# Kernel tuning notes

Measured on AMD Instinct MI355X. Metric: run time of the kernel, lower is better.

## Reference

```python
import jax, jax.numpy as jnp
import numpy as np

B, T, C = 2, 2048, 2048
N_HEAD = 16
HD = C // N_HEAD  # 128


def setup_inputs() -> dict:
    key = jax.random.key(0)
    k1, k2, k3, k4, k5 = jax.random.split(key, 5)
    s_in = 1.0 / np.sqrt(C)
    return {
        "x": jax.random.normal(k1, (B, T, C), dtype=jnp.float32),
        # weights stored as (in, out), i.e. transpose of torch Linear weight
        "W_attn": jax.random.normal(k2, (C, 3 * C), dtype=jnp.float32) * s_in,
        "b_attn": jax.random.normal(k3, (3 * C,), dtype=jnp.float32) * 0.02,
        "W_proj": jax.random.normal(k4, (C, C), dtype=jnp.float32) * s_in,
        "b_proj": jax.random.normal(k5, (C,), dtype=jnp.float32) * 0.02,
    }


def reference(x, W_attn, b_attn, W_proj, b_proj):
    # qkv projection: (B,T,3C)
    qkv = x @ W_attn + b_attn
    q, k, v = jnp.split(qkv, 3, axis=-1)
    # (B, n_head, T, head_dim)
    q = q.reshape(B, T, N_HEAD, HD).transpose(0, 2, 1, 3)
    k = k.reshape(B, T, N_HEAD, HD).transpose(0, 2, 1, 3)
    v = v.reshape(B, T, N_HEAD, HD).transpose(0, 2, 1, 3)
    # scores (B,H,T,T), causal mask (T_q == T_k prefill path)
    att = jnp.einsum("bhqd,bhkd->bhqk", q, k) * (1.0 / np.sqrt(HD))
    causal = jnp.tril(jnp.ones((T, T), dtype=bool))
    att = jnp.where(causal[None, None], att, -jnp.inf)
    att = jax.nn.softmax(att, axis=-1)  # attn_dropout is identity (p=0)
    y = jnp.einsum("bhqk,bhkd->bhqd", att, v)
    y = y.transpose(0, 2, 1, 3).reshape(B, T, C)
    y = y @ W_proj + b_proj  # resid_dropout identity (p=0)
    # new_cache = (k, v, T) since T == block_size; return output tensor
    return y
```

## Files before the change

kernel.cpp:

```cpp
#include <hip/hip_runtime.h>
#include <cstdint>
#include <cstddef>


typedef __bf16 bf16x8 __attribute__((ext_vector_type(8)));
typedef float  f32x4  __attribute__((ext_vector_type(4)));

__device__ __forceinline__ unsigned short f2bf(float f) {
  unsigned int u = __builtin_bit_cast(unsigned int, f);
  u += 0x7fffu + ((u >> 16) & 1u);
  return (unsigned short)(u >> 16);
}

__device__ __forceinline__ void gld16(void* lds, const void* g) {
  __builtin_amdgcn_global_load_lds(
      (const __attribute__((address_space(1))) void*)g,
      (__attribute__((address_space(3))) void*)lds, 16, 0, 0);
}

__global__ void cvt_f32_bf16_k(const float* __restrict__ in,
                               unsigned short* __restrict__ out, int n4) {
  int i = blockIdx.x * blockDim.x + threadIdx.x;
  int stride = gridDim.x * blockDim.x;
  for (; i < n4; i += stride) {
    float4 v = ((const float4*)in)[i];
    ushort4 o;
    o.x = f2bf(v.x); o.y = f2bf(v.y); o.z = f2bf(v.z); o.w = f2bf(v.w);
    ((ushort4*)out)[i] = o;
  }
}

__global__ void transpose_f32_bf16(const float* __restrict__ in,
                                   unsigned short* __restrict__ out,
                                   int R, int C) {
  __shared__ float tile[32][33];
  int c0 = blockIdx.x * 32, r0 = blockIdx.y * 32;
  int tx = threadIdx.x, ty = threadIdx.y;
#pragma unroll
  for (int i = 0; i < 4; i++)
    tile[ty + i * 8][tx] = in[(size_t)(r0 + ty + i * 8) * C + c0 + tx];
  __syncthreads();
#pragma unroll
  for (int i = 0; i < 4; i++)
    out[(size_t)(c0 + ty + i * 8) * R + r0 + tx] = f2bf(tile[tx][ty + i * 8]);
}

__global__ void extract_vT_k(const unsigned short* __restrict__ qkv,
                             unsigned short* __restrict__ vT) {
  __shared__ unsigned short tile[32][33];
  int bh = blockIdx.z;
  int b = bh >> 4, h = bh & 15;
  int t0 = blockIdx.x * 32, d0 = blockIdx.y * 32;
  int tx = threadIdx.x, ty = threadIdx.y;
  const unsigned short* src = qkv + (size_t)(b * 2048) * 6144 + 4096 + h * 128;
#pragma unroll
  for (int i = 0; i < 4; i++)
    tile[ty + i * 8][tx] = src[(size_t)(t0 + ty + i * 8) * 6144 + d0 + tx];
  __syncthreads();
  unsigned short* dst = vT + (size_t)bh * 128 * 2048;
#pragma unroll
  for (int i = 0; i < 4; i++)
    dst[(size_t)(d0 + ty + i * 8) * 2048 + t0 + tx] = tile[tx][ty + i * 8];
}

template <int OUT_BF16>
__global__ __launch_bounds__(256) void gemm_bt(
    const unsigned short* __restrict__ A, const unsigned short* __restrict__ BT,
    const float* __restrict__ bias, void* __restrict__ Cout,
    int M, int N, int K) {
  __shared__ __align__(16) unsigned short sA[128 * 32];
  __shared__ __align__(16) unsigned short sB[128 * 32];

  const int tid = threadIdx.x, w = tid >> 6, lane = tid & 63;
  const int quad = lane >> 4, l16 = lane & 15;
  const int m0 = blockIdx.y * 128, n0 = blockIdx.x * 128;
  const int wr = w >> 1, wc = w & 1;

  const int c0 = w * 128 + lane;
  const int c1 = w * 128 + 64 + lane;
  const unsigned short* gA0 = A + (size_t)(m0 + (c0 >> 2)) * K + (c0 & 3) * 8;
  const unsigned short* gA1 = A + (size_t)(m0 + (c1 >> 2)) * K + (c1 & 3) * 8;
  const unsigned short* gB0 = BT + (size_t)(n0 + (c0 >> 2)) * K + (c0 & 3) * 8;
  const unsigned short* gB1 = BT + (size_t)(n0 + (c1 >> 2)) * K + (c1 & 3) * 8;
  unsigned short* lA0 = sA + (size_t)(w * 128) * 8;
  unsigned short* lA1 = sA + (size_t)(w * 128 + 64) * 8;
  unsigned short* lB0 = sB + (size_t)(w * 128) * 8;
  unsigned short* lB1 = sB + (size_t)(w * 128 + 64) * 8;

  f32x4 acc[4][4] = {};

  for (int k0 = 0; k0 < K; k0 += 32) {
    gld16(lA0, gA0); gld16(lA1, gA1);
    gld16(lB0, gB0); gld16(lB1, gB1);
    gA0 += 32; gA1 += 32; gB0 += 32; gB1 += 32;
    __syncthreads();

    bf16x8 af[4], bfr[4];
#pragma unroll
    for (int mi = 0; mi < 4; mi++)
      af[mi] = *(const bf16x8*)&sA[(wr * 64 + mi * 16 + l16) * 32 + quad * 8];
#pragma unroll
    for (int ni = 0; ni < 4; ni++)
      bfr[ni] = *(const bf16x8*)&sB[(wc * 64 + ni * 16 + l16) * 32 + quad * 8];
#pragma unroll
    for (int mi = 0; mi < 4; mi++)
#pragma unroll
      for (int ni = 0; ni < 4; ni++)
        acc[mi][ni] = __builtin_amdgcn_mfma_f32_16x16x32_bf16(
            af[mi], bfr[ni], acc[mi][ni], 0, 0, 0);
    __syncthreads();
  }

#pragma unroll
  for (int mi = 0; mi < 4; mi++) {
    int row = m0 + wr * 64 + mi * 16 + quad * 4;
#pragma unroll
    for (int ni = 0; ni < 4; ni++) {
      int col = n0 + wc * 64 + ni * 16 + l16;
      float bv = bias[col];
#pragma unroll
      for (int r = 0; r < 4; r++) {
        float v = acc[mi][ni][r] + bv;
        if (OUT_BF16)
          ((unsigned short*)Cout)[(size_t)(row + r) * N + col] = f2bf(v);
        else
          ((float*)Cout)[(size_t)(row + r) * N + col] = v;
      }
    }
  }
}

__global__ __launch_bounds__(256) void flash_attn(
    const unsigned short* __restrict__ qkv, const unsigned short* __restrict__ vT,
    unsigned short* __restrict__ yout) {
  __shared__ __align__(16) unsigned short sK[2][64 * 128];
  __shared__ __align__(16) unsigned short sVT[2][128 * 64];
  __shared__ __align__(16) unsigned short sP[4 * 16 * 64];

  const int tid = threadIdx.x, w = tid >> 6, lane = tid & 63;
  const int quad = lane >> 4, l16 = lane & 15;
  const int id = blockIdx.x;
  const int g = id & 31;
  const int qp = id >> 5;
  const int b = g >> 4, h = g & 15;
  const int T = 2048, CC = 6144, HD = 128;
  const float qscale = 0.12753257252f;

  const unsigned short* gK = qkv + (size_t)(b * T) * CC + 2048 + h * HD;
  const unsigned short* gV = vT + (size_t)(b * 16 + h) * HD * T;
  unsigned short* pw = sP + w * 16 * 64;

  const unsigned short* kSrc[4];
  const unsigned short* vSrc[4];
  unsigned short* kDst[4];
  unsigned short* vDst[4];
#pragma unroll
  for (int i = 0; i < 4; i++) {
    int c = w * 256 + i * 64 + lane;
    int kR = c >> 4, kC = (c & 15) ^ (kR & 15);
    int vR = c >> 3, vC = (c & 7) ^ (vR & 7);
    kSrc[i] = gK + (size_t)kR * CC + kC * 8;
    vSrc[i] = gV + (size_t)vR * T + vC * 8;
    kDst[i] = (unsigned short*)sK + (size_t)(w * 256 + i * 64) * 8;
    vDst[i] = (unsigned short*)sVT + (size_t)(w * 256 + i * 64) * 8;
  }
  const int KBUF = 64 * 128, VBUF = 128 * 64;

  const int qtA = qp, qtB = 31 - qp;
  int qt = qtA, kt = 0;

  bf16x8 qf[4];
  float m_old[4], l_sum[4];
  f32x4 o[8] = {};
  {
    const size_t qrow = (size_t)(b * T + qt * 64 + w * 16 + l16) * CC + h * HD;
#pragma unroll
    for (int kb = 0; kb < 4; kb++) {
      bf16x8 raw = *(const bf16x8*)&qkv[qrow + kb * 32 + quad * 8];
      bf16x8 sc;
#pragma unroll
      for (int j = 0; j < 8; j++) sc[j] = (__bf16)((float)raw[j] * qscale);
      qf[kb] = sc;
    }
  }
#pragma unroll
  for (int r = 0; r < 4; r++) { m_old[r] = -1e30f; l_sum[r] = 0.f; }

#pragma unroll
  for (int i = 0; i < 4; i++) {
    gld16(kDst[i], kSrc[i]);
    gld16(vDst[i], vSrc[i]);
  }

  const int total = qtA + qtB + 2;
  for (int it = 0; it < total; ++it) {
    __syncthreads();
    const int cur = it & 1;
    const bool segEnd = (kt == qt);

    if (it + 1 < total) {
      const int nkt = segEnd ? 0 : kt + 1;
      const int nb_ = (it + 1) & 1;
      const size_t kOff = (size_t)nkt * 64 * CC;
      const int vOff = nkt * 64;
#pragma unroll
      for (int i = 0; i < 4; i++) {
        gld16(kDst[i] + (size_t)nb_ * KBUF * 8 / 8, kSrc[i] + kOff);
        gld16(vDst[i] + (size_t)nb_ * VBUF, vSrc[i] + vOff);
      }
    }

    const unsigned short* sKc = (const unsigned short*)sK + (size_t)cur * KBUF;
    const unsigned short* sVc = (const unsigned short*)sVT + (size_t)cur * VBUF;
    f32x4 s4[4] = {};
#pragma unroll
    for (int kb = 0; kb < 4; kb++) {
#pragma unroll
      for (int cb = 0; cb < 4; cb++) {
        int rr = cb * 16 + l16;
        int cc = (kb * 4 + quad) ^ l16;
        bf16x8 kf = *(const bf16x8*)&sKc[rr * 128 + cc * 8];
        s4[cb] = __builtin_amdgcn_mfma_f32_16x16x32_bf16(qf[kb], kf, s4[cb], 0, 0, 0);
      }
    }

    float sv[4][4];
#pragma unroll
    for (int cb = 0; cb < 4; cb++)
#pragma unroll
      for (int r = 0; r < 4; r++) {
        float v = s4[cb][r];
        if (segEnd) {
          int col = cb * 16 + l16;
          int row = w * 16 + quad * 4 + r;
          if (col > row) v = -1e30f;
        }
        sv[cb][r] = v;
      }

    float alpha[4];
#pragma unroll
    for (int r = 0; r < 4; r++) {
      float mx = fmaxf(fmaxf(sv[0][r], sv[1][r]), fmaxf(sv[2][r], sv[3][r]));
#pragma unroll
      for (int off = 8; off >= 1; off >>= 1) mx = fmaxf(mx, __shfl_xor(mx, off, 16));
      float m_new = fmaxf(m_old[r], mx);
      float a = exp2f(m_old[r] - m_new);
      float ssum = 0.f;
#pragma unroll
      for (int cb = 0; cb < 4; cb++) {
        float p = exp2f(sv[cb][r] - m_new);
        sv[cb][r] = p;
        ssum += p;
      }
#pragma unroll
      for (int off = 8; off >= 1; off >>= 1) ssum += __shfl_xor(ssum, off, 16);
      l_sum[r] = l_sum[r] * a + ssum;
      m_old[r] = m_new;
      alpha[r] = a;
    }

#pragma unroll
    for (int nb = 0; nb < 8; nb++)
#pragma unroll
      for (int r = 0; r < 4; r++) o[nb][r] *= alpha[r];

#pragma unroll
    for (int cb = 0; cb < 4; cb++) {
#pragma unroll
      for (int r = 0; r < 4; r++) {
        int prow = quad * 4 + r;
        int pcol = cb * 16 + l16;
        int pcc = (pcol >> 3) ^ (prow & 7);
        pw[prow * 64 + pcc * 8 + (pcol & 7)] = f2bf(sv[cb][r]);
      }
    }

#pragma unroll
    for (int kb2 = 0; kb2 < 2; kb2++) {
      int pcc = (kb2 * 4 + quad) ^ (l16 & 7);
      bf16x8 pf = *(const bf16x8*)&pw[l16 * 64 + pcc * 8];
#pragma unroll
      for (int nb = 0; nb < 8; nb++) {
        int rr = nb * 16 + l16;
        int cc = (kb2 * 4 + quad) ^ (rr & 7);
        bf16x8 vf = *(const bf16x8*)&sVc[rr * 64 + cc * 8];
        o[nb] = __builtin_amdgcn_mfma_f32_16x16x32_bf16(pf, vf, o[nb], 0, 0, 0);
      }
    }

    if (segEnd) {
#pragma unroll
      for (int r = 0; r < 4; r++) {
        float inv = 1.0f / l_sum[r];
        size_t orow = (size_t)(b * T + qt * 64 + w * 16 + quad * 4 + r) * 2048 + h * HD;
#pragma unroll
        for (int nb = 0; nb < 8; nb++)
          yout[orow + nb * 16 + l16] = f2bf(o[nb][r] * inv);
      }
      if (it + 1 < total) {
        qt = qtB;
        const size_t qrow = (size_t)(b * T + qt * 64 + w * 16 + l16) * CC + h * HD;
#pragma unroll
        for (int kb = 0; kb < 4; kb++) {
          bf16x8 raw = *(const bf16x8*)&qkv[qrow + kb * 32 + quad * 8];
          bf16x8 sc;
#pragma unroll
          for (int j = 0; j < 8; j++) sc[j] = (__bf16)((float)raw[j] * qscale);
          qf[kb] = sc;
        }
#pragma unroll
        for (int r = 0; r < 4; r++) { m_old[r] = -1e30f; l_sum[r] = 0.f; }
#pragma unroll
        for (int nb = 0; nb < 8; nb++) o[nb] = (f32x4){0.f, 0.f, 0.f, 0.f};
      }
      kt = 0;
    } else {
      kt++;
    }
  }
}

extern "C" void kernel_launch(void* const* d_in, const int* in_sizes, int n_in,
                              void* d_out, int out_size, void* d_ws, size_t ws_size,
                              hipStream_t stream) {
  const float* x      = (const float*)d_in[0];
  const float* W_attn = (const float*)d_in[1];
  const float* b_attn = (const float*)d_in[2];
  const float* W_proj = (const float*)d_in[3];
  const float* b_proj = (const float*)d_in[4];
  float* out = (float*)d_out;

  char* ws = (char*)d_ws;
  unsigned short* x_bf  = (unsigned short*)(ws);
  unsigned short* WaT   = (unsigned short*)(ws + 16777216);
  unsigned short* WpT   = (unsigned short*)(ws + 41943040);
  unsigned short* qkv   = (unsigned short*)(ws + 50331648);
  unsigned short* vT    = (unsigned short*)(ws + 100663296);
  unsigned short* y_att = (unsigned short*)(ws + 117440512);

  cvt_f32_bf16_k<<<1024, 256, 0, stream>>>(x, x_bf, 8388608 / 4);
  transpose_f32_bf16<<<dim3(192, 64), dim3(32, 8), 0, stream>>>(W_attn, WaT, 2048, 6144);
  transpose_f32_bf16<<<dim3(64, 64), dim3(32, 8), 0, stream>>>(W_proj, WpT, 2048, 2048);
  gemm_bt<1><<<dim3(48, 32), 256, 0, stream>>>(x_bf, WaT, b_attn, qkv, 4096, 6144, 2048);
  extract_vT_k<<<dim3(64, 4, 32), dim3(32, 8), 0, stream>>>(qkv, vT);
  flash_attn<<<dim3(512), 256, 0, stream>>>(qkv, vT, y_att);
  gemm_bt<0><<<dim3(16, 32), 256, 0, stream>>>(y_att, WpT, b_proj, out, 4096, 2048, 2048);
}
```

Before: 440.3 us.

## Widen GEMM K-tile with swizzled LDS, vectorize transposes, transpose S in attention

The GEMM now stages 64-wide K tiles through XOR-swizzled LDS, which halves the number of barriers per K and is meant to reduce bank conflicts. The weight-transpose and V-extract kernels move to 64x64 tiles with vectorized 16-byte global loads and stores. Flash attention computes S transposed (K as the A operand), so each lane owns one query row: the softmax reductions need only two cross-lane shuffles, and P is written to LDS as packed 4-element stores. The cost is extra shuffles to broadcast alpha and 1/l back to the row layout, plus more LDS per GEMM block.

```diff
diff --git a/kernel.cpp b/kernel.cpp
--- a/kernel.cpp
+++ b/kernel.cpp
@@ -5,6 +5,8 @@
 
 typedef __bf16 bf16x8 __attribute__((ext_vector_type(8)));
 typedef float  f32x4  __attribute__((ext_vector_type(4)));
+typedef unsigned short u16x4 __attribute__((ext_vector_type(4)));
+typedef unsigned short u16x8 __attribute__((ext_vector_type(8)));
 
 __device__ __forceinline__ unsigned short f2bf(float f) {
   unsigned int u = __builtin_bit_cast(unsigned int, f);
@@ -30,37 +32,62 @@
   }
 }
 
-__global__ void transpose_f32_bf16(const float* __restrict__ in,
-                                   unsigned short* __restrict__ out,
-                                   int R, int C) {
-  __shared__ float tile[32][33];
-  int c0 = blockIdx.x * 32, r0 = blockIdx.y * 32;
-  int tx = threadIdx.x, ty = threadIdx.y;
-#pragma unroll
-  for (int i = 0; i < 4; i++)
-    tile[ty + i * 8][tx] = in[(size_t)(r0 + ty + i * 8) * C + c0 + tx];
+__global__ __launch_bounds__(256) void transpose_f32_bf16(
+    const float* __restrict__ in, unsigned short* __restrict__ out,
+    int R, int C) {
+  __shared__ float tile[64][65];
+  int c0 = blockIdx.x * 64, r0 = blockIdx.y * 64;
+  int t = threadIdx.x;
+  int lr = t >> 4, lc = (t & 15) * 4;
+#pragma unroll
+  for (int i = 0; i < 4; i++) {
+    int row = lr + i * 16;
+    float4 v = *(const float4*)&in[(size_t)(r0 + row) * C + c0 + lc];
+    tile[row][lc] = v.x; tile[row][lc + 1] = v.y;
+    tile[row][lc + 2] = v.z; tile[row][lc + 3] = v.w;
+  }
   __syncthreads();
-#pragma unroll
-  for (int i = 0; i < 4; i++)
-    out[(size_t)(c0 + ty + i * 8) * R + r0 + tx] = f2bf(tile[tx][ty + i * 8]);
-}
-
-__global__ void extract_vT_k(const unsigned short* __restrict__ qkv,
-                             unsigned short* __restrict__ vT) {
-  __shared__ unsigned short tile[32][33];
-  int bh = blockIdx.z;
-  int b = bh >> 4, h = bh & 15;
-  int t0 = blockIdx.x * 32, d0 = blockIdx.y * 32;
-  int tx = threadIdx.x, ty = threadIdx.y;
+  int wr = t >> 3, wc = (t & 7) * 8;
+#pragma unroll
+  for (int i = 0; i < 2; i++) {
+    int crow = wr + i * 32;
+    u16x8 o;
+#pragma unroll
+    for (int j = 0; j < 8; j++) o[j] = f2bf(tile[wc + j][crow]);
+    *(u16x8*)&out[(size_t)(c0 + crow) * R + r0 + wc] = o;
+  }
+}
+
+__global__ __launch_bounds__(256) void extract_vT_k(
+    const unsigned short* __restrict__ qkv, unsigned short* __restrict__ vT) {
+  __shared__ unsigned int tile32[64][33];
+  int bh = blockIdx.z, b = bh >> 4, h = bh & 15;
+  int t0 = blockIdx.x * 64, d0 = blockIdx.y * 64;
+  int t = threadIdx.x;
+  int lr = t >> 3, lc = (t & 7) * 8;
   const unsigned short* src = qkv + (size_t)(b * 2048) * 6144 + 4096 + h * 128;
 #pragma unroll
-  for (int i = 0; i < 4; i++)
-    tile[ty + i * 8][tx] = src[(size_t)(t0 + ty + i * 8) * 6144 + d0 + tx];
+  for (int i = 0; i < 2; i++) {
+    int row = lr + i * 32;
+    u16x8 v = *(const u16x8*)&src[(size_t)(t0 + row) * 6144 + d0 + lc];
+#pragma unroll
+    for (int j = 0; j < 8; j++) {
+      unsigned short* p = (unsigned short*)&tile32[lc + j][row & 31];
+      p[row >> 5] = v[j];
+    }
+  }
   __syncthreads();
-  unsigned short* dst = vT + (size_t)bh * 128 * 2048;
-#pragma unroll
-  for (int i = 0; i < 4; i++)
-    dst[(size_t)(d0 + ty + i * 8) * 2048 + t0 + tx] = tile[tx][ty + i * 8];
+  int dr = t >> 2, tc = (t & 3) * 8;
+  u16x8 lo, hi;
+#pragma unroll
+  for (int j = 0; j < 8; j++) {
+    unsigned int u = tile32[dr][tc + j];
+    lo[j] = (unsigned short)(u & 0xffffu);
+    hi[j] = (unsigned short)(u >> 16);
+  }
+  unsigned short* dst = vT + (size_t)bh * 128 * 2048 + (size_t)(d0 + dr) * 2048 + t0;
+  *(u16x8*)&dst[tc] = lo;
+  *(u16x8*)&dst[tc + 32] = hi;
 }
 
 template <int OUT_BF16>
@@ -68,46 +95,55 @@
     const unsigned short* __restrict__ A, const unsigned short* __restrict__ BT,
     const float* __restrict__ bias, void* __restrict__ Cout,
     int M, int N, int K) {
-  __shared__ __align__(16) unsigned short sA[128 * 32];
-  __shared__ __align__(16) unsigned short sB[128 * 32];
+  __shared__ __align__(16) unsigned short sA[128 * 64];
+  __shared__ __align__(16) unsigned short sB[128 * 64];
 
   const int tid = threadIdx.x, w = tid >> 6, lane = tid & 63;
   const int quad = lane >> 4, l16 = lane & 15;
   const int m0 = blockIdx.y * 128, n0 = blockIdx.x * 128;
   const int wr = w >> 1, wc = w & 1;
 
-  const int c0 = w * 128 + lane;
-  const int c1 = w * 128 + 64 + lane;
-  const unsigned short* gA0 = A + (size_t)(m0 + (c0 >> 2)) * K + (c0 & 3) * 8;
-  const unsigned short* gA1 = A + (size_t)(m0 + (c1 >> 2)) * K + (c1 & 3) * 8;
-  const unsigned short* gB0 = BT + (size_t)(n0 + (c0 >> 2)) * K + (c0 & 3) * 8;
-  const unsigned short* gB1 = BT + (size_t)(n0 + (c1 >> 2)) * K + (c1 & 3) * 8;
-  unsigned short* lA0 = sA + (size_t)(w * 128) * 8;
-  unsigned short* lA1 = sA + (size_t)(w * 128 + 64) * 8;
-  unsigned short* lB0 = sB + (size_t)(w * 128) * 8;
-  unsigned short* lB1 = sB + (size_t)(w * 128 + 64) * 8;
+  const unsigned short* gA[4];
+  const unsigned short* gB[4];
+  unsigned short* lA[4];
+  unsigned short* lB[4];
+#pragma unroll
+  for (int i = 0; i < 4; i++) {
+    int c = w * 256 + i * 64 + lane;
+    int row = c >> 3, scol = (c & 7) ^ (row & 7);
+    gA[i] = A + (size_t)(m0 + row) * K + scol * 8;
+    gB[i] = BT + (size_t)(n0 + row) * K + scol * 8;
+    lA[i] = sA + (size_t)(w * 256 + i * 64) * 8;
+    lB[i] = sB + (size_t)(w * 256 + i * 64) * 8;
+  }
 
   f32x4 acc[4][4] = {};
 
-  for (int k0 = 0; k0 < K; k0 += 32) {
-    gld16(lA0, gA0); gld16(lA1, gA1);
-    gld16(lB0, gB0); gld16(lB1, gB1);
-    gA0 += 32; gA1 += 32; gB0 += 32; gB1 += 32;
+  for (int k0 = 0; k0 < K; k0 += 64) {
+#pragma unroll
+    for (int i = 0; i < 4; i++) {
+      gld16(lA[i], gA[i]); gld16(lB[i], gB[i]);
+      gA[i] += 64; gB[i] += 64;
+    }
     __syncthreads();
 
-    bf16x8 af[4], bfr[4];
-#pragma unroll
-    for (int mi = 0; mi < 4; mi++)
-      af[mi] = *(const bf16x8*)&sA[(wr * 64 + mi * 16 + l16) * 32 + quad * 8];
-#pragma unroll
-    for (int ni = 0; ni < 4; ni++)
-      bfr[ni] = *(const bf16x8*)&sB[(wc * 64 + ni * 16 + l16) * 32 + quad * 8];
-#pragma unroll
-    for (int mi = 0; mi < 4; mi++)
+#pragma unroll
+    for (int kk = 0; kk < 2; kk++) {
+      const int cc = (kk * 4 + quad) ^ (l16 & 7);
+      bf16x8 af[4], bfr[4];
+#pragma unroll
+      for (int mi = 0; mi < 4; mi++)
+        af[mi] = *(const bf16x8*)&sA[(wr * 64 + mi * 16 + l16) * 64 + cc * 8];
 #pragma unroll
       for (int ni = 0; ni < 4; ni++)
-        acc[mi][ni] = __builtin_amdgcn_mfma_f32_16x16x32_bf16(
-            af[mi], bfr[ni], acc[mi][ni], 0, 0, 0);
+        bfr[ni] = *(const bf16x8*)&sB[(wc * 64 + ni * 16 + l16) * 64 + cc * 8];
+#pragma unroll
+      for (int mi = 0; mi < 4; mi++)
+#pragma unroll
+        for (int ni = 0; ni < 4; ni++)
+          acc[mi][ni] = __builtin_amdgcn_mfma_f32_16x16x32_bf16(
+              af[mi], bfr[ni], acc[mi][ni], 0, 0, 0);
+    }
     __syncthreads();
   }
 
@@ -170,7 +206,7 @@
   int qt = qtA, kt = 0;
 
   bf16x8 qf[4];
-  float m_old[4], l_sum[4];
+  float m_old, l_sum;
   f32x4 o[8] = {};
   {
     const size_t qrow = (size_t)(b * T + qt * 64 + w * 16 + l16) * CC + h * HD;
@@ -183,8 +219,7 @@
       qf[kb] = sc;
     }
   }
-#pragma unroll
-  for (int r = 0; r < 4; r++) { m_old[r] = -1e30f; l_sum[r] = 0.f; }
+  m_old = -1e30f; l_sum = 0.f;
 
 #pragma unroll
   for (int i = 0; i < 4; i++) {
@@ -205,75 +240,78 @@
       const int vOff = nkt * 64;
 #pragma unroll
       for (int i = 0; i < 4; i++) {
-        gld16(kDst[i] + (size_t)nb_ * KBUF * 8 / 8, kSrc[i] + kOff);
+        gld16(kDst[i] + (size_t)nb_ * KBUF, kSrc[i] + kOff);
         gld16(vDst[i] + (size_t)nb_ * VBUF, vSrc[i] + vOff);
       }
     }
 
     const unsigned short* sKc = (const unsigned short*)sK + (size_t)cur * KBUF;
     const unsigned short* sVc = (const unsigned short*)sVT + (size_t)cur * VBUF;
+
     f32x4 s4[4] = {};
 #pragma unroll
+    for (int dc = 0; dc < 4; dc++) {
+#pragma unroll
+      for (int kb = 0; kb < 4; kb++) {
+        int rr = kb * 16 + l16;
+        int cc = (dc * 4 + quad) ^ l16;
+        bf16x8 kf = *(const bf16x8*)&sKc[rr * 128 + cc * 8];
+        s4[kb] = __builtin_amdgcn_mfma_f32_16x16x32_bf16(kf, qf[dc], s4[kb], 0, 0, 0);
+      }
+    }
+
+    float sv[4][4];
+#pragma unroll
+    for (int kb = 0; kb < 4; kb++)
+#pragma unroll
+      for (int r = 0; r < 4; r++) {
+        float v = s4[kb][r];
+        if (segEnd) {
+          if (kb * 16 + quad * 4 + r > w * 16 + l16) v = -1e30f;
+        }
+        sv[kb][r] = v;
+      }
+
+    float mx = sv[0][0];
+#pragma unroll
+    for (int kb = 0; kb < 4; kb++)
+#pragma unroll
+      for (int r = 0; r < 4; r++) mx = fmaxf(mx, sv[kb][r]);
+    mx = fmaxf(mx, __shfl_xor(mx, 16));
+    mx = fmaxf(mx, __shfl_xor(mx, 32));
+    float m_new = fmaxf(m_old, mx);
+    float a = exp2f(m_old - m_new);
+    float ssum = 0.f;
+#pragma unroll
+    for (int kb = 0; kb < 4; kb++)
+#pragma unroll
+      for (int r = 0; r < 4; r++) {
+        float p = exp2f(sv[kb][r] - m_new);
+        sv[kb][r] = p;
+        ssum += p;
+      }
+    ssum += __shfl_xor(ssum, 16);
+    ssum += __shfl_xor(ssum, 32);
+    l_sum = l_sum * a + ssum;
+    m_old = m_new;
+
+    float ar[4];
+#pragma unroll
+    for (int r = 0; r < 4; r++)
+      ar[r] = __shfl(a, (lane & 48) + quad * 4 + r);
+#pragma unroll
+    for (int nb = 0; nb < 8; nb++)
+#pragma unroll
+      for (int r = 0; r < 4; r++) o[nb][r] *= ar[r];
+
+#pragma unroll
     for (int kb = 0; kb < 4; kb++) {
-#pragma unroll
-      for (int cb = 0; cb < 4; cb++) {
-        int rr = cb * 16 + l16;
-        int cc = (kb * 4 + quad) ^ l16;
-        bf16x8 kf = *(const bf16x8*)&sKc[rr * 128 + cc * 8];
-        s4[cb] = __builtin_amdgcn_mfma_f32_16x16x32_bf16(qf[kb], kf, s4[cb], 0, 0, 0);
-      }
-    }
-
-    float sv[4][4];
-#pragma unroll
-    for (int cb = 0; cb < 4; cb++)
-#pragma unroll
-      for (int r = 0; r < 4; r++) {
-        float v = s4[cb][r];
-        if (segEnd) {
-          int col = cb * 16 + l16;
-          int row = w * 16 + quad * 4 + r;
-          if (col > row) v = -1e30f;
-        }
-        sv[cb][r] = v;
-      }
-
-    float alpha[4];
-#pragma unroll
-    for (int r = 0; r < 4; r++) {
-      float mx = fmaxf(fmaxf(sv[0][r], sv[1][r]), fmaxf(sv[2][r], sv[3][r]));
-#pragma unroll
-      for (int off = 8; off >= 1; off >>= 1) mx = fmaxf(mx, __shfl_xor(mx, off, 16));
-      float m_new = fmaxf(m_old[r], mx);
-      float a = exp2f(m_old[r] - m_new);
-      float ssum = 0.f;
-#pragma unroll
-      for (int cb = 0; cb < 4; cb++) {
-        float p = exp2f(sv[cb][r] - m_new);
-        sv[cb][r] = p;
-        ssum += p;
-      }
-#pragma unroll
-      for (int off = 8; off >= 1; off >>= 1) ssum += __shfl_xor(ssum, off, 16);
-      l_sum[r] = l_sum[r] * a + ssum;
-      m_old[r] = m_new;
-      alpha[r] = a;
-    }
-
-#pragma unroll
-    for (int nb = 0; nb < 8; nb++)
-#pragma unroll
-      for (int r = 0; r < 4; r++) o[nb][r] *= alpha[r];
-
-#pragma unroll
-    for (int cb = 0; cb < 4; cb++) {
-#pragma unroll
-      for (int r = 0; r < 4; r++) {
-        int prow = quad * 4 + r;
-        int pcol = cb * 16 + l16;
-        int pcc = (pcol >> 3) ^ (prow & 7);
-        pw[prow * 64 + pcc * 8 + (pcol & 7)] = f2bf(sv[cb][r]);
-      }
+      u16x4 pk;
+#pragma unroll
+      for (int r = 0; r < 4; r++) pk[r] = f2bf(sv[kb][r]);
+      int c = kb * 2 + (quad >> 1);
+      int cp = c ^ (l16 & 7);
+      *(u16x4*)&pw[l16 * 64 + cp * 8 + (quad & 1) * 4] = pk;
     }
 
 #pragma unroll
@@ -290,13 +328,14 @@
     }
 
     if (segEnd) {
+      float linv = 1.0f / l_sum;
 #pragma unroll
       for (int r = 0; r < 4; r++) {
-        float inv = 1.0f / l_sum[r];
+        float ir = __shfl(linv, (lane & 48) + quad * 4 + r);
         size_t orow = (size_t)(b * T + qt * 64 + w * 16 + quad * 4 + r) * 2048 + h * HD;
 #pragma unroll
         for (int nb = 0; nb < 8; nb++)
-          yout[orow + nb * 16 + l16] = f2bf(o[nb][r] * inv);
+          yout[orow + nb * 16 + l16] = f2bf(o[nb][r] * ir);
       }
       if (it + 1 < total) {
         qt = qtB;
@@ -309,8 +348,7 @@
           for (int j = 0; j < 8; j++) sc[j] = (__bf16)((float)raw[j] * qscale);
           qf[kb] = sc;
         }
-#pragma unroll
-        for (int r = 0; r < 4; r++) { m_old[r] = -1e30f; l_sum[r] = 0.f; }
+        m_old = -1e30f; l_sum = 0.f;
 #pragma unroll
         for (int nb = 0; nb < 8; nb++) o[nb] = (f32x4){0.f, 0.f, 0.f, 0.f};
       }
@@ -340,10 +378,10 @@
   unsigned short* y_att = (unsigned short*)(ws + 117440512);
 
   cvt_f32_bf16_k<<<1024, 256, 0, stream>>>(x, x_bf, 8388608 / 4);
-  transpose_f32_bf16<<<dim3(192, 64), dim3(32, 8), 0, stream>>>(W_attn, WaT, 2048, 6144);
-  transpose_f32_bf16<<<dim3(64, 64), dim3(32, 8), 0, stream>>>(W_proj, WpT, 2048, 2048);
+  transpose_f32_bf16<<<dim3(96, 32), 256, 0, stream>>>(W_attn, WaT, 2048, 6144);
+  transpose_f32_bf16<<<dim3(32, 32), 256, 0, stream>>>(W_proj, WpT, 2048, 2048);
   gemm_bt<1><<<dim3(48, 32), 256, 0, stream>>>(x_bf, WaT, b_attn, qkv, 4096, 6144, 2048);
-  extract_vT_k<<<dim3(64, 4, 32), dim3(32, 8), 0, stream>>>(qkv, vT);
+  extract_vT_k<<<dim3(32, 2, 32), 256, 0, stream>>>(qkv, vT);
   flash_attn<<<dim3(512), 256, 0, stream>>>(qkv, vT, y_att);
   gemm_bt<0><<<dim3(16, 32), 256, 0, stream>>>(y_att, WpT, b_proj, out, 4096, 2048, 2048);
 }
```

Result: faster. 386.9 us (-12.1%).
